# Kernel optimization log

Measured on AMD Instinct MI355X. Metric: run time of the kernel, lower is better.

Reference implementation:

```python
import jax, jax.numpy as jnp
import numpy as np

DIM, KEY_DIM, HEADS, RATIO, RES = 384, 32, 8, 4, 14
NH_KD = KEY_DIM * HEADS            # 256
D = RATIO * KEY_DIM                # 128
DH = D * HEADS                     # 1024
H_QKV = DH + 2 * NH_KD             # 1536
N_OFF = RES * RES                  # 196 unique (|dy|,|dx|) offsets
EPS = 1e-5


def _bn(x, g, b, m, v):
    # inference-mode BatchNorm2d over channel dim 1 of [B,C,H,W]
    s = (g * jax.lax.rsqrt(v + EPS))[None, :, None, None]
    return x * s + (b - m * g * jax.lax.rsqrt(v + EPS))[None, :, None, None]


def setup_inputs() -> dict:
    key = jax.random.key(0)
    ks = jax.random.split(key, 8)
    B = 256
    x = jax.random.normal(ks[0], (B, DIM, RES, RES), dtype=jnp.float32)
    # 1x1 qkv conv weight [out,in]
    qkv_w = jax.random.normal(ks[1], (H_QKV, DIM), dtype=jnp.float32) * 0.02
    # depthwise 3x3 conv on q channels [C,1,3,3]
    dw_w = jax.random.normal(ks[2], (NH_KD, 1, 3, 3), dtype=jnp.float32) * 0.1
    # 1x1 proj conv weight [out,in]
    proj_w = jax.random.normal(ks[3], (DIM, DH), dtype=jnp.float32) * 0.02
    attention_biases = jax.random.normal(ks[4], (HEADS, N_OFF), dtype=jnp.float32) * 0.1

    def bn_params(k, c):
        k1, k2 = jax.random.split(k)
        return (1.0 + 0.1 * jax.random.normal(k1, (c,), dtype=jnp.float32),
                0.1 * jax.random.normal(k2, (c,), dtype=jnp.float32),
                jnp.zeros((c,), jnp.float32), jnp.ones((c,), jnp.float32))
    qkv_g, qkv_b, qkv_m, qkv_v = bn_params(ks[5], H_QKV)
    dw_g, dw_b, dw_m, dw_v = bn_params(ks[6], NH_KD)
    proj_g, proj_b, proj_m, proj_v = bn_params(ks[7], DIM)

    # relative position bias index map [N, N], via (|dy|, |dx|) -> |dy|*RES + |dx|
    pts = np.arange(RES)
    yy, xx = np.meshgrid(pts, pts, indexing='ij')
    coords = np.stack([yy.ravel(), xx.ravel()], axis=1)  # [N,2]
    dy = np.abs(coords[:, None, 0] - coords[None, :, 0])
    dx = np.abs(coords[:, None, 1] - coords[None, :, 1])
    bias_idxs = jnp.asarray(dy * RES + dx, dtype=jnp.int32)  # [N,N]

    return dict(x=x, qkv_w=qkv_w, qkv_g=qkv_g, qkv_b=qkv_b, qkv_m=qkv_m, qkv_v=qkv_v,
                dw_w=dw_w, dw_g=dw_g, dw_b=dw_b, dw_m=dw_m, dw_v=dw_v,
                proj_w=proj_w, proj_g=proj_g, proj_b=proj_b, proj_m=proj_m, proj_v=proj_v,
                attention_biases=attention_biases, bias_idxs=bias_idxs)


def reference(x, qkv_w, qkv_g, qkv_b, qkv_m, qkv_v,
              dw_w, dw_g, dw_b, dw_m, dw_v,
              proj_w, proj_g, proj_b, proj_m, proj_v,
              attention_biases, bias_idxs):
    B, _, Hs, Ws = x.shape
    N = Hs * Ws
    scale = KEY_DIM ** -0.5
    # qkv: 1x1 conv + BN
    qkv = _bn(jnp.einsum('bchw,oc->bohw', x, qkv_w), qkv_g, qkv_b, qkv_m, qkv_v)
    q, k, v = jnp.split(qkv, [NH_KD, 2 * NH_KD], axis=1)
    # depthwise 3x3 conv + BN on q
    q = jax.lax.conv_general_dilated(q, dw_w, (1, 1), 'SAME',
                                     feature_group_count=NH_KD,
                                     dimension_numbers=('NCHW', 'OIHW', 'NCHW'))
    q = _bn(q, dw_g, dw_b, dw_m, dw_v)
    q = q.reshape(B, HEADS, KEY_DIM, N)
    k = k.reshape(B, HEADS, KEY_DIM, N)
    v = v.reshape(B, HEADS, D, N)
    ab = attention_biases[:, bias_idxs]                     # [heads, N, N]
    attn = jnp.einsum('bhdn,bhdm->bhnm', q, k) * scale + ab[None]
    attn = jax.nn.softmax(attn, axis=-1)
    out = jnp.einsum('bhdm,bhnm->bhdn', v, attn).reshape(B, DH, Hs, Ws)
    # proj: ReLU -> 1x1 conv -> BN
    out = jnp.einsum('bchw,oc->bohw', jax.nn.relu(out), proj_w)
    out = _bn(out, proj_g, proj_b, proj_m, proj_v)
    return out
```

## Files before the change

kernel.cpp:

```cpp
#include <hip/hip_runtime.h>
#include <hip/hip_bf16.h>
#include <stdint.h>

#define DIM 384
#define KEY_DIM 32
#define HEADS 8
#define RES 14
#define NTOK 196
#define NH_KD 256
#define DD 128
#define DHF 1024
#define H_QKV 1536
#define BATCH 256
#define QSTR 224
#define EPS_BN 1e-5f
#define SCALE_QK 0.17677669529663687f

typedef unsigned short ushort_t;
typedef __attribute__((ext_vector_type(8))) short short8;
typedef __attribute__((ext_vector_type(4))) float floatx4;

__device__ __forceinline__ ushort_t f2bf(float f) {
  union { float f; unsigned int u; } v; v.f = f;
  unsigned int u = v.u;
  unsigned int r = (u + 0x7FFFu + ((u >> 16) & 1u)) >> 16;
  return (ushort_t)r;
}
__device__ __forceinline__ float bf2f(ushort_t h) {
  union { unsigned int u; float f; } v; v.u = ((unsigned int)h) << 16;
  return v.f;
}
__device__ __forceinline__ void async_copy16(const ushort_t* g, ushort_t* l) {
  __builtin_amdgcn_global_load_lds((const __attribute__((address_space(1))) void*)g,
                                   (__attribute__((address_space(3))) void*)l, 16, 0, 0);
}

__global__ void k_prep_x(const float* __restrict__ x, ushort_t* __restrict__ xb) {
  __shared__ float tile[64][65];
  const int b = blockIdx.y;
  const int c0 = blockIdx.x * 64;
  const int t = threadIdx.x;
  const int tr = t >> 6;
  const int tc = t & 63;
  for (int n0 = 0; n0 < NTOK; n0 += 64) {
    __syncthreads();
    #pragma unroll
    for (int k = 0; k < 16; ++k) {
      int r = k * 4 + tr;
      int n = n0 + tc;
      tile[r][tc] = (n < NTOK) ? x[((size_t)b * DIM + c0 + r) * NTOK + n] : 0.f;
    }
    __syncthreads();
    #pragma unroll
    for (int k = 0; k < 16; ++k) {
      int nl = k * 4 + tr;
      int n = n0 + nl;
      if (n < NTOK) xb[((size_t)b * NTOK + n) * DIM + c0 + tc] = f2bf(tile[tc][nl]);
    }
  }
}

__global__ void k_prep_w(const float* __restrict__ qkv_w, const float* __restrict__ proj_w,
                         ushort_t* __restrict__ wqkvb, ushort_t* __restrict__ wprojb) {
  int i = blockIdx.x * 256 + threadIdx.x;
  const int nA = H_QKV * DIM;
  const int nB = DIM * DHF;
  if (i < nA) wqkvb[i] = f2bf(qkv_w[i]);
  else if (i < nA + nB) wprojb[i - nA] = f2bf(proj_w[i - nA]);
}

__global__ void k_prep_ab(const float* __restrict__ biases, const int* __restrict__ idxs,
                          float* __restrict__ abg) {
  int i = blockIdx.x * 256 + threadIdx.x;
  if (i >= HEADS * NTOK * NTOK) return;
  int h = i / (NTOK * NTOK);
  int nm = i - h * (NTOK * NTOK);
  abg[i] = biases[h * NTOK + idxs[nm]];
}

template<int KDIM, bool OUTF32>
__global__ __launch_bounds__(256, 2) void k_gemm(
    const ushort_t* __restrict__ A, const ushort_t* __restrict__ B,
    const float* __restrict__ bn_g, const float* __restrict__ bn_b,
    const float* __restrict__ bn_m, const float* __restrict__ bn_v,
    void* __restrict__ out) {
  __shared__ ushort_t sA[128 * 32];
  __shared__ ushort_t sB[128 * 32];
  const int b = blockIdx.y;
  const int ot = blockIdx.x >> 1;
  const int nt = blockIdx.x & 1;
  const int o0 = ot * 128;
  const int n0 = nt * 128;
  const int t = threadIdx.x;
  const int w = t >> 6;
  const int l = t & 63;
  const int lr = l >> 2;
  const int ls = l & 3;
  const int arow0 = w * 32 + lr;
  const int arow1 = arow0 + 16;
  const size_t aoff0 = (size_t)(o0 + arow0) * KDIM + ls * 8;
  const size_t aoff1 = (size_t)(o0 + arow1) * KDIM + ls * 8;
  int bn0 = n0 + arow0; if (bn0 > NTOK - 1) bn0 = NTOK - 1;
  int bn1 = n0 + arow1; if (bn1 > NTOK - 1) bn1 = NTOK - 1;
  const size_t boff0 = ((size_t)b * NTOK + bn0) * KDIM + ls * 8;
  const size_t boff1 = ((size_t)b * NTOK + bn1) * KDIM + ls * 8;
  ushort_t* sA_w = sA + w * 1024;
  ushort_t* sB_w = sB + w * 1024;

  floatx4 acc[4][4];
  const floatx4 zero4 = {0.f, 0.f, 0.f, 0.f};
  #pragma unroll
  for (int i = 0; i < 4; ++i)
    #pragma unroll
    for (int j = 0; j < 4; ++j) acc[i][j] = zero4;

  const int wr = (w >> 1) * 64;
  const int wc = (w & 1) * 64;
  const int quad = l >> 4;
  const int l15 = l & 15;

  for (int kk = 0; kk < KDIM; kk += 32) {
    __syncthreads();
    async_copy16(A + aoff0 + kk, sA_w);
    async_copy16(A + aoff1 + kk, sA_w + 512);
    async_copy16(B + boff0 + kk, sB_w);
    async_copy16(B + boff1 + kk, sB_w + 512);
    __syncthreads();
    short8 af[4], bfv[4];
    #pragma unroll
    for (int i = 0; i < 4; ++i)
      af[i] = *(const short8*)(sA + (wr + i * 16 + l15) * 32 + quad * 8);
    #pragma unroll
    for (int j = 0; j < 4; ++j)
      bfv[j] = *(const short8*)(sB + (wc + j * 16 + l15) * 32 + quad * 8);
    #pragma unroll
    for (int i = 0; i < 4; ++i)
      #pragma unroll
      for (int j = 0; j < 4; ++j)
        acc[i][j] = __builtin_amdgcn_mfma_f32_16x16x32_bf16(af[i], bfv[j], acc[i][j], 0, 0, 0);
  }

  #pragma unroll
  for (int i = 0; i < 4; ++i) {
    #pragma unroll
    for (int r = 0; r < 4; ++r) {
      const int o = o0 + wr + i * 16 + quad * 4 + r;
      const float s = bn_g[o] * rsqrtf(bn_v[o] + EPS_BN);
      const float tt = bn_b[o] - bn_m[o] * s;
      #pragma unroll
      for (int j = 0; j < 4; ++j) {
        const int n = n0 + wc + j * 16 + l15;
        if (n < NTOK) {
          const float val = acc[i][j][r] * s + tt;
          if (OUTF32)
            ((float*)out)[((size_t)b * DIM + o) * NTOK + n] = val;
          else
            ((ushort_t*)out)[((size_t)b * H_QKV + o) * QSTR + n] = f2bf(val);
        }
      }
    }
  }
}

__global__ __launch_bounds__(64) void k_dwq(
    const ushort_t* __restrict__ qkvb, const float* __restrict__ dw_w,
    const float* __restrict__ dg, const float* __restrict__ db,
    const float* __restrict__ dm, const float* __restrict__ dv,
    ushort_t* __restrict__ qt, ushort_t* __restrict__ kt) {
  __shared__ ushort_t sq[32 * QSTR];
  __shared__ ushort_t sk[32 * QSTR];
  const int bh = blockIdx.x;
  const int b = bh >> 3, h = bh & 7;
  const int l = threadIdx.x;
  const int d = l & 31;
  const int half = l >> 5;
  const int c = h * 32 + d;
  float wv[9];
  #pragma unroll
  for (int tp = 0; tp < 9; ++tp) wv[tp] = dw_w[c * 9 + tp];
  const float s = dg[c] * rsqrtf(dv[c] + EPS_BN);
  const float tt = db[c] - dm[c] * s;
  const uint4* gq = (const uint4*)(qkvb + ((size_t)b * H_QKV + h * 32) * QSTR);
  const uint4* gk = (const uint4*)(qkvb + ((size_t)b * H_QKV + NH_KD + h * 32) * QSTR);
  uint4* lq = (uint4*)sq;
  uint4* lk = (uint4*)sk;
  for (int i = l; i < 896; i += 64) { lq[i] = gq[i]; lk[i] = gk[i]; }
  __syncthreads();
  for (int i = 0; i < 98; ++i) {
    const int n = i * 2 + half;
    const int y = n / 14, x = n - y * 14;
    float a = 0.f;
    #pragma unroll
    for (int dy = -1; dy <= 1; ++dy)
      #pragma unroll
      for (int dx = -1; dx <= 1; ++dx) {
        const int yy = y + dy, xx = x + dx;
        if (yy >= 0 && yy < 14 && xx >= 0 && xx < 14)
          a += bf2f(sq[d * QSTR + yy * 14 + xx]) * wv[(dy + 1) * 3 + (dx + 1)];
      }
    const float outv = (a * s + tt) * SCALE_QK;
    qt[((size_t)bh * NTOK + n) * 32 + d] = f2bf(outv);
    kt[((size_t)bh * NTOK + n) * 32 + d] = sk[d * QSTR + n];
  }
}

__global__ __launch_bounds__(256, 2) void k_attn(
    const ushort_t* __restrict__ qt, const ushort_t* __restrict__ kt,
    const ushort_t* __restrict__ qkvb, const float* __restrict__ abg,
    ushort_t* __restrict__ rbuf) {
  __shared__ ushort_t sK[208 * 32];
  __shared__ ushort_t sP[4 * 16 * 224];
  __shared__ ushort_t sO[4 * 16 * 128];
  const int bh = blockIdx.x;
  const int b = bh >> 3, h = bh & 7;
  const int t = threadIdx.x;
  const int w = t >> 6, l = t & 63;
  const int quad = l >> 4, l15 = l & 15;

  {
    const uint4* gk = (const uint4*)(kt + (size_t)bh * NTOK * 32);
    uint4* lk = (uint4*)sK;
    for (int i = t; i < 784; i += 256) lk[i] = gk[i];
    const uint4 z = make_uint4(0, 0, 0, 0);
    if (t < 48) lk[784 + t] = z;
    if (t < 128) {
      const int wb = t >> 5, rr = (t >> 1) & 15, hf = t & 1;
      *(uint4*)(sP + wb * 3584 + rr * 224 + 208 + hf * 8) = z;
    }
  }
  __syncthreads();

  const ushort_t* qbase = qt + (size_t)bh * NTOK * 32;
  const ushort_t* vbase = qkvb + ((size_t)b * H_QKV + 2 * NH_KD + h * DD) * QSTR;
  ushort_t* myP = sP + w * (16 * 224);
  ushort_t* myO = sO + w * (16 * 128);
  const floatx4 zero4 = {0.f, 0.f, 0.f, 0.f};

  for (int rt = w; rt < 13; rt += 4) {
    int qrow = rt * 16 + l15; if (qrow > NTOK - 1) qrow = NTOK - 1;
    const short8 aq = *(const short8*)(qbase + qrow * 32 + quad * 8);
    floatx4 lg[13];
    #pragma unroll
    for (int j = 0; j < 13; ++j) {
      const short8 bk = *(const short8*)(sK + (j * 16 + l15) * 32 + quad * 8);
      lg[j] = __builtin_amdgcn_mfma_f32_16x16x32_bf16(aq, bk, zero4, 0, 0, 0);
    }
    float mx[4] = {-3e38f, -3e38f, -3e38f, -3e38f};
    #pragma unroll
    for (int r = 0; r < 4; ++r) {
      int n = rt * 16 + quad * 4 + r; if (n > NTOK - 1) n = NTOK - 1;
      const float* abrow = abg + ((size_t)h * NTOK + n) * NTOK;
      #pragma unroll
      for (int j = 0; j < 13; ++j) {
        const int m = j * 16 + l15;
        float v = lg[j][r];
        v = (m < NTOK) ? (v + abrow[m]) : -1e30f;
        lg[j][r] = v;
        mx[r] = fmaxf(mx[r], v);
      }
    }
    #pragma unroll
    for (int r = 0; r < 4; ++r) {
      float m = mx[r];
      m = fmaxf(m, __shfl_xor(m, 1));
      m = fmaxf(m, __shfl_xor(m, 2));
      m = fmaxf(m, __shfl_xor(m, 4));
      m = fmaxf(m, __shfl_xor(m, 8));
      mx[r] = m;
    }
    float sum[4] = {0.f, 0.f, 0.f, 0.f};
    #pragma unroll
    for (int j = 0; j < 13; ++j)
      #pragma unroll
      for (int r = 0; r < 4; ++r) {
        const float e = __expf(lg[j][r] - mx[r]);
        lg[j][r] = e;
        sum[r] += e;
      }
    #pragma unroll
    for (int r = 0; r < 4; ++r) {
      float sv = sum[r];
      sv += __shfl_xor(sv, 1);
      sv += __shfl_xor(sv, 2);
      sv += __shfl_xor(sv, 4);
      sv += __shfl_xor(sv, 8);
      sum[r] = 1.f / sv;
    }
    #pragma unroll
    for (int j = 0; j < 13; ++j)
      #pragma unroll
      for (int r = 0; r < 4; ++r)
        myP[(quad * 4 + r) * 224 + j * 16 + l15] = f2bf(lg[j][r] * sum[r]);

    short8 aA[7];
    #pragma unroll
    for (int ks = 0; ks < 7; ++ks)
      aA[ks] = *(const short8*)(myP + l15 * 224 + ks * 32 + quad * 8);
    #pragma unroll
    for (int ct = 0; ct < 8; ++ct) {
      floatx4 a = zero4;
      #pragma unroll
      for (int ks = 0; ks < 7; ++ks) {
        const short8 bv = *(const short8*)(vbase + (size_t)(ct * 16 + l15) * QSTR + ks * 32 + quad * 8);
        a = __builtin_amdgcn_mfma_f32_16x16x32_bf16(aA[ks], bv, a, 0, 0, 0);
      }
      #pragma unroll
      for (int r = 0; r < 4; ++r) {
        const float v = a[r];
        myO[(quad * 4 + r) * 128 + ct * 16 + l15] = f2bf(v > 0.f ? v : 0.f);
      }
    }
    #pragma unroll
    for (int p = 0; p < 4; ++p) {
      const int nl = p * 4 + quad;
      const int n = rt * 16 + nl;
      const uint4 val = *(const uint4*)(myO + nl * 128 + l15 * 8);
      if (n < NTOK)
        *(uint4*)(rbuf + ((size_t)b * NTOK + n) * DHF + h * DD + l15 * 8) = val;
    }
  }
}

extern "C" void kernel_launch(void* const* d_in, const int* in_sizes, int n_in,
                              void* d_out, int out_size, void* d_ws, size_t ws_size,
                              hipStream_t stream) {
  const float* x      = (const float*)d_in[0];
  const float* qkv_w  = (const float*)d_in[1];
  const float* qkv_g  = (const float*)d_in[2];
  const float* qkv_b  = (const float*)d_in[3];
  const float* qkv_m  = (const float*)d_in[4];
  const float* qkv_v  = (const float*)d_in[5];
  const float* dw_w   = (const float*)d_in[6];
  const float* dw_g   = (const float*)d_in[7];
  const float* dw_b   = (const float*)d_in[8];
  const float* dw_m   = (const float*)d_in[9];
  const float* dw_v   = (const float*)d_in[10];
  const float* proj_w = (const float*)d_in[11];
  const float* proj_g = (const float*)d_in[12];
  const float* proj_b = (const float*)d_in[13];
  const float* proj_m = (const float*)d_in[14];
  const float* proj_v = (const float*)d_in[15];
  const float* ab     = (const float*)d_in[16];
  const int*   idxs   = (const int*)d_in[17];
  (void)in_sizes; (void)n_in; (void)out_size;

  char* p = (char*)d_ws;
  ushort_t* wqkvb  = (ushort_t*)p; p += (size_t)H_QKV * DIM * 2;
  ushort_t* wprojb = (ushort_t*)p; p += (size_t)DIM * DHF * 2;
  float*    abg    = (float*)p;    p += (size_t)HEADS * NTOK * NTOK * 4;
  const size_t fixed = (size_t)(p - (char*)d_ws);
  const size_t perb = (size_t)NTOK * DIM * 2 + (size_t)H_QKV * QSTR * 2
                    + 2 * (size_t)HEADS * NTOK * 32 * 2 + (size_t)NTOK * DHF * 2;
  int cb = 8;
  const int cands[6] = {256, 128, 64, 32, 16, 8};
  for (int i = 0; i < 6; ++i) {
    if (fixed + (size_t)cands[i] * perb <= ws_size) { cb = cands[i]; break; }
  }
  ushort_t* xb   = (ushort_t*)p;
  ushort_t* qkvb = xb + (size_t)cb * NTOK * DIM;
  ushort_t* qt   = qkvb + (size_t)cb * H_QKV * QSTR;
  ushort_t* kt   = qt + (size_t)cb * HEADS * NTOK * 32;
  ushort_t* rbuf = kt + (size_t)cb * HEADS * NTOK * 32;

  k_prep_w<<<(H_QKV * DIM + DIM * DHF + 255) / 256, 256, 0, stream>>>(qkv_w, proj_w, wqkvb, wprojb);
  k_prep_ab<<<(HEADS * NTOK * NTOK + 255) / 256, 256, 0, stream>>>(ab, idxs, abg);

  for (int b0 = 0; b0 < BATCH; b0 += cb) {
    k_prep_x<<<dim3(6, cb), 256, 0, stream>>>(x + (size_t)b0 * DIM * NTOK, xb);
    k_gemm<DIM, false><<<dim3(24, cb), 256, 0, stream>>>(wqkvb, xb, qkv_g, qkv_b, qkv_m, qkv_v, qkvb);
    k_dwq<<<cb * HEADS, 64, 0, stream>>>(qkvb, dw_w, dw_g, dw_b, dw_m, dw_v, qt, kt);
    k_attn<<<cb * HEADS, 256, 0, stream>>>(qt, kt, qkvb, abg, rbuf);
    k_gemm<DHF, true><<<dim3(6, cb), 256, 0, stream>>>(wprojb, rbuf, proj_g, proj_b, proj_m, proj_v,
                                                       (float*)d_out + (size_t)b0 * DIM * NTOK);
  }
}
```

Measured before the change: 795.3 us.

## Pad tokens to 224 for batched GEMM tiles, split attention by V halves, prelayout bias

Pads the per-image token dimension to 224 so both 1x1-conv GEMMs tile the flattened batch*token axis with no wasted half-empty 128-column tiles. The attention kernel is split into two blocks per (batch, head), one per half of V's channels. Each block stages its V slice in LDS, keeps the K fragments in registers, and injects a pre-laid-out, log2e-scaled bias directly as the MFMA accumulator init. exp2 replaces exp, with log2e folded into the q scale. In exchange, the QK^T and softmax work is duplicated across the two halves, and the padded rows add extra workspace and GEMM work.

```diff
diff --git a/kernel.cpp b/kernel.cpp
--- a/kernel.cpp
+++ b/kernel.cpp
@@ -14,7 +14,9 @@
 #define BATCH 256
 #define QSTR 224
 #define EPS_BN 1e-5f
-#define SCALE_QK 0.17677669529663687f
+#define LOG2E 1.4426950408889634f
+#define QSCALE 0.25501860152f
+#define PSTR 232
 
 typedef unsigned short ushort_t;
 typedef __attribute__((ext_vector_type(8))) short short8;
@@ -42,7 +44,7 @@
   const int t = threadIdx.x;
   const int tr = t >> 6;
   const int tc = t & 63;
-  for (int n0 = 0; n0 < NTOK; n0 += 64) {
+  for (int n0 = 0; n0 < QSTR; n0 += 64) {
     __syncthreads();
     #pragma unroll
     for (int k = 0; k < 16; ++k) {
@@ -55,7 +57,7 @@
     for (int k = 0; k < 16; ++k) {
       int nl = k * 4 + tr;
       int n = n0 + nl;
-      if (n < NTOK) xb[((size_t)b * NTOK + n) * DIM + c0 + tc] = f2bf(tile[tc][nl]);
+      if (n < QSTR) xb[((size_t)b * QSTR + n) * DIM + c0 + tc] = f2bf(tile[tc][nl]);
     }
   }
 }
@@ -69,13 +71,23 @@
   else if (i < nA + nB) wprojb[i - nA] = f2bf(proj_w[i - nA]);
 }
 
-__global__ void k_prep_ab(const float* __restrict__ biases, const int* __restrict__ idxs,
-                          float* __restrict__ abg) {
-  int i = blockIdx.x * 256 + threadIdx.x;
-  if (i >= HEADS * NTOK * NTOK) return;
-  int h = i / (NTOK * NTOK);
-  int nm = i - h * (NTOK * NTOK);
-  abg[i] = biases[h * NTOK + idxs[nm]];
+__global__ void k_prep_abC(const float* __restrict__ biases, const int* __restrict__ idxs,
+                           float* __restrict__ abgC) {
+  int tid = blockIdx.x * 256 + threadIdx.x;
+  if (tid >= HEADS * 13 * 13 * 64) return;
+  const int l = tid & 63;
+  int rem = tid >> 6;
+  const int j = rem % 13; rem /= 13;
+  const int rt = rem % 13;
+  const int h = rem / 13;
+  const int quad = l >> 4, l15 = l & 15;
+  const int m = j * 16 + l15;
+  #pragma unroll
+  for (int r = 0; r < 4; ++r) {
+    int n = rt * 16 + quad * 4 + r; if (n > NTOK - 1) n = NTOK - 1;
+    float v = (m < NTOK) ? biases[h * NTOK + idxs[n * NTOK + m]] * LOG2E : -1e30f;
+    abgC[(size_t)tid * 4 + r] = v;
+  }
 }
 
 template<int KDIM, bool OUTF32>
@@ -86,24 +98,18 @@
     void* __restrict__ out) {
   __shared__ ushort_t sA[128 * 32];
   __shared__ ushort_t sB[128 * 32];
-  const int b = blockIdx.y;
-  const int ot = blockIdx.x >> 1;
-  const int nt = blockIdx.x & 1;
-  const int o0 = ot * 128;
-  const int n0 = nt * 128;
+  const int n0 = blockIdx.x * 128;
+  const int o0 = blockIdx.y * 128;
   const int t = threadIdx.x;
   const int w = t >> 6;
   const int l = t & 63;
   const int lr = l >> 2;
   const int ls = l & 3;
   const int arow0 = w * 32 + lr;
-  const int arow1 = arow0 + 16;
   const size_t aoff0 = (size_t)(o0 + arow0) * KDIM + ls * 8;
-  const size_t aoff1 = (size_t)(o0 + arow1) * KDIM + ls * 8;
-  int bn0 = n0 + arow0; if (bn0 > NTOK - 1) bn0 = NTOK - 1;
-  int bn1 = n0 + arow1; if (bn1 > NTOK - 1) bn1 = NTOK - 1;
-  const size_t boff0 = ((size_t)b * NTOK + bn0) * KDIM + ls * 8;
-  const size_t boff1 = ((size_t)b * NTOK + bn1) * KDIM + ls * 8;
+  const size_t aoff1 = aoff0 + (size_t)16 * KDIM;
+  const size_t boff0 = (size_t)(n0 + arow0) * KDIM + ls * 8;
+  const size_t boff1 = boff0 + (size_t)16 * KDIM;
   ushort_t* sA_w = sA + w * 1024;
   ushort_t* sB_w = sB + w * 1024;
 
@@ -140,6 +146,13 @@
         acc[i][j] = __builtin_amdgcn_mfma_f32_16x16x32_bf16(af[i], bfv[j], acc[i][j], 0, 0, 0);
   }
 
+  unsigned bq[4], nn[4];
+  #pragma unroll
+  for (int j = 0; j < 4; ++j) {
+    const unsigned gn = n0 + wc + j * 16 + l15;
+    bq[j] = gn / QSTR;
+    nn[j] = gn - bq[j] * QSTR;
+  }
   #pragma unroll
   for (int i = 0; i < 4; ++i) {
     #pragma unroll
@@ -149,13 +162,12 @@
       const float tt = bn_b[o] - bn_m[o] * s;
       #pragma unroll
       for (int j = 0; j < 4; ++j) {
-        const int n = n0 + wc + j * 16 + l15;
-        if (n < NTOK) {
-          const float val = acc[i][j][r] * s + tt;
-          if (OUTF32)
-            ((float*)out)[((size_t)b * DIM + o) * NTOK + n] = val;
-          else
-            ((ushort_t*)out)[((size_t)b * H_QKV + o) * QSTR + n] = f2bf(val);
+        const float val = acc[i][j][r] * s + tt;
+        if (OUTF32) {
+          if (nn[j] < NTOK)
+            ((float*)out)[((size_t)bq[j] * DIM + o) * NTOK + nn[j]] = val;
+        } else {
+          ((ushort_t*)out)[((size_t)bq[j] * H_QKV + o) * QSTR + nn[j]] = f2bf(val);
         }
       }
     }
@@ -198,7 +210,7 @@
         if (yy >= 0 && yy < 14 && xx >= 0 && xx < 14)
           a += bf2f(sq[d * QSTR + yy * 14 + xx]) * wv[(dy + 1) * 3 + (dx + 1)];
       }
-    const float outv = (a * s + tt) * SCALE_QK;
+    const float outv = (a * s + tt) * QSCALE;
     qt[((size_t)bh * NTOK + n) * 32 + d] = f2bf(outv);
     kt[((size_t)bh * NTOK + n) * 32 + d] = sk[d * QSTR + n];
   }
@@ -206,59 +218,57 @@
 
 __global__ __launch_bounds__(256, 2) void k_attn(
     const ushort_t* __restrict__ qt, const ushort_t* __restrict__ kt,
-    const ushort_t* __restrict__ qkvb, const float* __restrict__ abg,
+    const ushort_t* __restrict__ qkvb, const float* __restrict__ abgC,
     ushort_t* __restrict__ rbuf) {
-  __shared__ ushort_t sK[208 * 32];
-  __shared__ ushort_t sP[4 * 16 * 224];
-  __shared__ ushort_t sO[4 * 16 * 128];
-  const int bh = blockIdx.x;
+  __shared__ ushort_t sV[64 * PSTR];
+  __shared__ ushort_t sP[4 * 16 * PSTR];
+  const int id = blockIdx.x;
+  const int dhalf = id & 1;
+  const int bh = id >> 1;
   const int b = bh >> 3, h = bh & 7;
   const int t = threadIdx.x;
   const int w = t >> 6, l = t & 63;
   const int quad = l >> 4, l15 = l & 15;
 
   {
-    const uint4* gk = (const uint4*)(kt + (size_t)bh * NTOK * 32);
-    uint4* lk = (uint4*)sK;
-    for (int i = t; i < 784; i += 256) lk[i] = gk[i];
-    const uint4 z = make_uint4(0, 0, 0, 0);
-    if (t < 48) lk[784 + t] = z;
+    const ushort_t* vsrc = qkvb + ((size_t)b * H_QKV + 2 * NH_KD + h * DD + dhalf * 64) * QSTR;
+    for (int i = t; i < 2048; i += 256) {
+      const int row = i >> 5, col = i & 31;
+      if (col < 28)
+        *(uint4*)(sV + row * PSTR + col * 8) = *(const uint4*)(vsrc + (size_t)row * QSTR + col * 8);
+    }
     if (t < 128) {
       const int wb = t >> 5, rr = (t >> 1) & 15, hf = t & 1;
-      *(uint4*)(sP + wb * 3584 + rr * 224 + 208 + hf * 8) = z;
-    }
+      *(uint4*)(sP + wb * 16 * PSTR + rr * PSTR + 208 + hf * 8) = make_uint4(0, 0, 0, 0);
+    }
+  }
+  short8 kf[13];
+  const ushort_t* kbase = kt + (size_t)bh * NTOK * 32;
+  #pragma unroll
+  for (int j = 0; j < 13; ++j) {
+    int krow = j * 16 + l15; if (krow > NTOK - 1) krow = NTOK - 1;
+    kf[j] = *(const short8*)(kbase + krow * 32 + quad * 8);
   }
   __syncthreads();
 
   const ushort_t* qbase = qt + (size_t)bh * NTOK * 32;
-  const ushort_t* vbase = qkvb + ((size_t)b * H_QKV + 2 * NH_KD + h * DD) * QSTR;
-  ushort_t* myP = sP + w * (16 * 224);
-  ushort_t* myO = sO + w * (16 * 128);
+  ushort_t* myP = sP + w * 16 * PSTR;
   const floatx4 zero4 = {0.f, 0.f, 0.f, 0.f};
 
   for (int rt = w; rt < 13; rt += 4) {
     int qrow = rt * 16 + l15; if (qrow > NTOK - 1) qrow = NTOK - 1;
     const short8 aq = *(const short8*)(qbase + qrow * 32 + quad * 8);
+    const floatx4* cb = (const floatx4*)(abgC) + ((size_t)(h * 13 + rt) * 13) * 64 + l;
     floatx4 lg[13];
     #pragma unroll
-    for (int j = 0; j < 13; ++j) {
-      const short8 bk = *(const short8*)(sK + (j * 16 + l15) * 32 + quad * 8);
-      lg[j] = __builtin_amdgcn_mfma_f32_16x16x32_bf16(aq, bk, zero4, 0, 0, 0);
-    }
+    for (int j = 0; j < 13; ++j)
+      lg[j] = __builtin_amdgcn_mfma_f32_16x16x32_bf16(aq, kf[j], cb[j * 64], 0, 0, 0);
+
     float mx[4] = {-3e38f, -3e38f, -3e38f, -3e38f};
     #pragma unroll
-    for (int r = 0; r < 4; ++r) {
-      int n = rt * 16 + quad * 4 + r; if (n > NTOK - 1) n = NTOK - 1;
-      const float* abrow = abg + ((size_t)h * NTOK + n) * NTOK;
-      #pragma unroll
-      for (int j = 0; j < 13; ++j) {
-        const int m = j * 16 + l15;
-        float v = lg[j][r];
-        v = (m < NTOK) ? (v + abrow[m]) : -1e30f;
-        lg[j][r] = v;
-        mx[r] = fmaxf(mx[r], v);
-      }
-    }
+    for (int j = 0; j < 13; ++j)
+      #pragma unroll
+      for (int r = 0; r < 4; ++r) mx[r] = fmaxf(mx[r], lg[j][r]);
     #pragma unroll
     for (int r = 0; r < 4; ++r) {
       float m = mx[r];
@@ -273,7 +283,7 @@
     for (int j = 0; j < 13; ++j)
       #pragma unroll
       for (int r = 0; r < 4; ++r) {
-        const float e = __expf(lg[j][r] - mx[r]);
+        const float e = exp2f(lg[j][r] - mx[r]);
         lg[j][r] = e;
         sum[r] += e;
       }
@@ -290,33 +300,34 @@
     for (int j = 0; j < 13; ++j)
       #pragma unroll
       for (int r = 0; r < 4; ++r)
-        myP[(quad * 4 + r) * 224 + j * 16 + l15] = f2bf(lg[j][r] * sum[r]);
+        myP[(quad * 4 + r) * PSTR + j * 16 + l15] = f2bf(lg[j][r] * sum[r]);
 
     short8 aA[7];
     #pragma unroll
     for (int ks = 0; ks < 7; ++ks)
-      aA[ks] = *(const short8*)(myP + l15 * 224 + ks * 32 + quad * 8);
-    #pragma unroll
-    for (int ct = 0; ct < 8; ++ct) {
+      aA[ks] = *(const short8*)(myP + l15 * PSTR + ks * 32 + quad * 8);
+    #pragma unroll
+    for (int ct = 0; ct < 4; ++ct) {
       floatx4 a = zero4;
       #pragma unroll
       for (int ks = 0; ks < 7; ++ks) {
-        const short8 bv = *(const short8*)(vbase + (size_t)(ct * 16 + l15) * QSTR + ks * 32 + quad * 8);
+        const short8 bv = *(const short8*)(sV + (ct * 16 + l15) * PSTR + ks * 32 + quad * 8);
         a = __builtin_amdgcn_mfma_f32_16x16x32_bf16(aA[ks], bv, a, 0, 0, 0);
       }
       #pragma unroll
       for (int r = 0; r < 4; ++r) {
         const float v = a[r];
-        myO[(quad * 4 + r) * 128 + ct * 16 + l15] = f2bf(v > 0.f ? v : 0.f);
+        myP[(quad * 4 + r) * PSTR + ct * 16 + l15] = f2bf(v > 0.f ? v : 0.f);
       }
     }
     #pragma unroll
     for (int p = 0; p < 4; ++p) {
       const int nl = p * 4 + quad;
       const int n = rt * 16 + nl;
-      const uint4 val = *(const uint4*)(myO + nl * 128 + l15 * 8);
-      if (n < NTOK)
-        *(uint4*)(rbuf + ((size_t)b * NTOK + n) * DHF + h * DD + l15 * 8) = val;
+      if (n < NTOK) {
+        const uint2 val = *(const uint2*)(myP + nl * PSTR + l15 * 4);
+        *(uint2*)(rbuf + ((size_t)b * QSTR + n) * DHF + h * DD + dhalf * 64 + l15 * 4) = val;
+      }
     }
   }
 }
@@ -347,30 +358,31 @@
   char* p = (char*)d_ws;
   ushort_t* wqkvb  = (ushort_t*)p; p += (size_t)H_QKV * DIM * 2;
   ushort_t* wprojb = (ushort_t*)p; p += (size_t)DIM * DHF * 2;
-  float*    abg    = (float*)p;    p += (size_t)HEADS * NTOK * NTOK * 4;
+  float*    abgC   = (float*)p;    p += (size_t)HEADS * 13 * 13 * 64 * 4 * 4;
   const size_t fixed = (size_t)(p - (char*)d_ws);
-  const size_t perb = (size_t)NTOK * DIM * 2 + (size_t)H_QKV * QSTR * 2
-                    + 2 * (size_t)HEADS * NTOK * 32 * 2 + (size_t)NTOK * DHF * 2;
+  const size_t perb = (size_t)QSTR * DIM * 2 + (size_t)H_QKV * QSTR * 2
+                    + 2 * (size_t)HEADS * NTOK * 32 * 2 + (size_t)QSTR * DHF * 2;
   int cb = 8;
   const int cands[6] = {256, 128, 64, 32, 16, 8};
   for (int i = 0; i < 6; ++i) {
     if (fixed + (size_t)cands[i] * perb <= ws_size) { cb = cands[i]; break; }
   }
   ushort_t* xb   = (ushort_t*)p;
-  ushort_t* qkvb = xb + (size_t)cb * NTOK * DIM;
+  ushort_t* qkvb = xb + (size_t)cb * QSTR * DIM;
   ushort_t* qt   = qkvb + (size_t)cb * H_QKV * QSTR;
   ushort_t* kt   = qt + (size_t)cb * HEADS * NTOK * 32;
   ushort_t* rbuf = kt + (size_t)cb * HEADS * NTOK * 32;
 
   k_prep_w<<<(H_QKV * DIM + DIM * DHF + 255) / 256, 256, 0, stream>>>(qkv_w, proj_w, wqkvb, wprojb);
-  k_prep_ab<<<(HEADS * NTOK * NTOK + 255) / 256, 256, 0, stream>>>(ab, idxs, abg);
-
+  k_prep_abC<<<(HEADS * 13 * 13 * 64 + 255) / 256, 256, 0, stream>>>(ab, idxs, abgC);
+
+  const int NT = cb * QSTR / 128;
   for (int b0 = 0; b0 < BATCH; b0 += cb) {
     k_prep_x<<<dim3(6, cb), 256, 0, stream>>>(x + (size_t)b0 * DIM * NTOK, xb);
-    k_gemm<DIM, false><<<dim3(24, cb), 256, 0, stream>>>(wqkvb, xb, qkv_g, qkv_b, qkv_m, qkv_v, qkvb);
+    k_gemm<DIM, false><<<dim3(NT, 12), 256, 0, stream>>>(wqkvb, xb, qkv_g, qkv_b, qkv_m, qkv_v, qkvb);
     k_dwq<<<cb * HEADS, 64, 0, stream>>>(qkvb, dw_w, dw_g, dw_b, dw_m, dw_v, qt, kt);
-    k_attn<<<cb * HEADS, 256, 0, stream>>>(qt, kt, qkvb, abg, rbuf);
-    k_gemm<DHF, true><<<dim3(6, cb), 256, 0, stream>>>(wprojb, rbuf, proj_g, proj_b, proj_m, proj_v,
+    k_attn<<<cb * HEADS * 2, 256, 0, stream>>>(qt, kt, qkvb, abgC, rbuf);
+    k_gemm<DHF, true><<<dim3(NT, 3), 256, 0, stream>>>(wprojb, rbuf, proj_g, proj_b, proj_m, proj_v,
                                                        (float*)d_out + (size_t)b0 * DIM * NTOK);
   }
 }
```

After: 685.8 us. 13.8% less time.
